# Kernel optimization log

Measured on AMD Instinct MI355X. Metric: run time of the kernel, lower is better.

The kernel has to match this reference:

```python
import jax, jax.numpy as jnp
import numpy as np

B, N, D, H = 4, 2048, 256, 8
d = D // H          # 32 per-head dim
EPS = 1e-5
SCALE = 1.0 / float(np.sqrt(d))


def setup_inputs() -> dict:
    key = jax.random.key(0)
    ks = jax.random.split(key, 6)
    s = 0.02
    x = jax.random.normal(ks[0], (B, N, D), jnp.float32)
    # RoPE frequencies: theta_j = 10000^(-2j/d), angle = pos * theta
    inv_freq = 1.0 / (10000.0 ** (jnp.arange(0, d, 2, dtype=jnp.float32) / d))  # (d/2,)
    ang = jnp.arange(N, dtype=jnp.float32)[:, None] * inv_freq[None, :]          # (N, d/2)
    return {
        "x": x,
        "freqs_cos": jnp.cos(ang),
        "freqs_sin": jnp.sin(ang),
        "w_qkv": jax.random.normal(ks[1], (D, 3 * D), jnp.float32) * s,
        "b_qkv": jnp.zeros((3 * D,), jnp.float32),
        "w_proj": jax.random.normal(ks[2], (D, D), jnp.float32) * s,
        "b_proj": jnp.zeros((D,), jnp.float32),
        "ln1_g": jnp.ones((D,), jnp.float32),
        "ln1_b": jnp.zeros((D,), jnp.float32),
        "ln2_g": jnp.ones((D,), jnp.float32),
        "ln2_b": jnp.zeros((D,), jnp.float32),
        "w1": jax.random.normal(ks[3], (D, 2 * D), jnp.float32) * s,
        "b1": jnp.zeros((2 * D,), jnp.float32),
        "w2": jax.random.normal(ks[4], (2 * D, D), jnp.float32) * s,
        "b2": jnp.zeros((D,), jnp.float32),
    }


def _layer_norm(x, g, b):
    mu = jnp.mean(x, axis=-1, keepdims=True)
    var = jnp.mean(jnp.square(x - mu), axis=-1, keepdims=True)
    return (x - mu) * jax.lax.rsqrt(var + EPS) * g + b


def _rope(t, cos, sin):
    # t: (B,H,N,d); interleaved (even,odd) pairs viewed as complex, multiplied by e^{i*ang}
    tr = t.reshape(B, H, N, d // 2, 2)
    te, to = tr[..., 0], tr[..., 1]
    c = cos[None, None, :, :]
    s = sin[None, None, :, :]
    oe = te * c - to * s
    oo = te * s + to * c
    return jnp.stack([oe, oo], axis=-1).reshape(B, H, N, d)


def reference(x, freqs_cos, freqs_sin, w_qkv, b_qkv, w_proj, b_proj,
              ln1_g, ln1_b, ln2_g, ln2_b, w1, b1, w2, b2):
    # Pre-LN MHSA with RoPE (dropout = identity at eval)
    h = _layer_norm(x, ln1_g, ln1_b)
    qkv = (h @ w_qkv + b_qkv).reshape(B, N, 3, H, d).transpose(0, 2, 3, 1, 4)  # (B,3,H,N,d)
    q, k, v = qkv[:, 0], qkv[:, 1], qkv[:, 2]
    q = _rope(q, freqs_cos, freqs_sin)
    k = _rope(k, freqs_cos, freqs_sin)
    attn = jax.nn.softmax(jnp.einsum('bhnd,bhmd->bhnm', q, k) * SCALE, axis=-1)
    out = jnp.einsum('bhnm,bhmd->bhnd', attn, v).transpose(0, 2, 1, 3).reshape(B, N, D)
    x = x + (out @ w_proj + b_proj)
    h = _layer_norm(x, ln2_g, ln2_b)
    ffn = jax.nn.relu(h @ w1 + b1) @ w2 + b2
    return x + ffn
```

## Files before the change

### kernel.cpp

```cpp
#include <hip/hip_runtime.h>
#include <hip/hip_bf16.h>
#include <math.h>

#define Bsz 4
#define Nseq 2048
#define Dm 256
#define Hh 8
#define Hd 32
#define EPS_ 1e-5f
#define SCALE_ 0.17677669529663687f
#define QSC_ (0.17677669529663687f * 1.4426950408889634f)

typedef __attribute__((ext_vector_type(8))) short short8;
typedef __attribute__((ext_vector_type(4))) short short4v;
typedef __attribute__((ext_vector_type(4))) float f32x4;
typedef __attribute__((ext_vector_type(16))) float f32x16;

__device__ __forceinline__ void gload16(const void* g, void* l) {
    __builtin_amdgcn_global_load_lds(
        (const __attribute__((address_space(1))) void*)g,
        (__attribute__((address_space(3))) void*)l, 16, 0, 0);
}

__device__ __forceinline__ short bf16s(float f) {
    __hip_bfloat16 h = __float2bfloat16(f);
    return *(short*)&h;
}

union FU { float f; unsigned u; };

__device__ __forceinline__ int pk2bf(float a, float b) {
    FU ua, ub; ua.f = a; ub.f = b;
    return (int)__builtin_amdgcn_perm(ub.u, ua.u, 0x07060302u);
}

union I4S8 { int i[4]; short8 s; };

__global__ __launch_bounds__(256) void prep_kernel(
    const float* __restrict__ x, const float* __restrict__ g1,
    const float* __restrict__ b1v, __hip_bfloat16* __restrict__ hout,
    const float* __restrict__ s0, const float* __restrict__ s1,
    const float* __restrict__ s2, const float* __restrict__ s3,
    __hip_bfloat16* __restrict__ d0, __hip_bfloat16* __restrict__ d1,
    __hip_bfloat16* __restrict__ d2, __hip_bfloat16* __restrict__ d3) {
    __shared__ float t[32][33];
    if (blockIdx.x < 2048) {
        int row  = blockIdx.x * 4 + (threadIdx.x >> 6);
        int lane = threadIdx.x & 63;
        const float* xr = x + (size_t)row * Dm;
        float4 v = *(const float4*)(xr + lane * 4);
        float s  = v.x + v.y + v.z + v.w;
        float ss = v.x * v.x + v.y * v.y + v.z * v.z + v.w * v.w;
        #pragma unroll
        for (int off = 32; off; off >>= 1) {
            s  += __shfl_xor(s, off);
            ss += __shfl_xor(ss, off);
        }
        float mu  = s * (1.0f / Dm);
        float var = ss * (1.0f / Dm) - mu * mu;
        float rs  = rsqrtf(var + EPS_);
        float4 gv = *(const float4*)(g1 + lane * 4);
        float4 bv = *(const float4*)(b1v + lane * 4);
        short4v o4 = { bf16s((v.x - mu) * rs * gv.x + bv.x),
                       bf16s((v.y - mu) * rs * gv.y + bv.y),
                       bf16s((v.z - mu) * rs * gv.z + bv.z),
                       bf16s((v.w - mu) * rs * gv.w + bv.w) };
        *(short4v*)(hout + (size_t)row * Dm + lane * 4) = o4;
        return;
    }
    int bid = blockIdx.x - 2048;
    const float* src; __hip_bfloat16* dst; int K, N, tb;
    if (bid < 192)      { src = s0; dst = d0; K = 256; N = 768; tb = bid; }
    else if (bid < 256) { src = s1; dst = d1; K = 256; N = 256; tb = bid - 192; }
    else if (bid < 384) { src = s2; dst = d2; K = 256; N = 512; tb = bid - 256; }
    else                { src = s3; dst = d3; K = 512; N = 256; tb = bid - 384; }
    int tn = N >> 5;
    int k0 = (tb / tn) * 32, n0 = (tb % tn) * 32;
    int c = threadIdx.x & 31, r0 = threadIdx.x >> 5;
    #pragma unroll
    for (int i = 0; i < 4; i++) {
        int r = r0 + i * 8;
        t[r][c] = src[(size_t)(k0 + r) * N + n0 + c];
    }
    __syncthreads();
    #pragma unroll
    for (int i = 0; i < 4; i++) {
        int n = r0 + i * 8;
        dst[(size_t)(n0 + n) * K + k0 + c] = __float2bfloat16(t[c][n]);
    }
}

__global__ __launch_bounds__(256) void qkv_mfma(const __hip_bfloat16* __restrict__ A,
                                                const __hip_bfloat16* __restrict__ Wt,
                                                const float* __restrict__ bias,
                                                const float* __restrict__ fcos,
                                                const float* __restrict__ fsin,
                                                __hip_bfloat16* __restrict__ qout,
                                                __hip_bfloat16* __restrict__ kout,
                                                __hip_bfloat16* __restrict__ vt) {
    const int K = 256;
    __shared__ __align__(16) __hip_bfloat16 As[2][64 * 64];
    __shared__ __align__(16) __hip_bfloat16 Bs[2][64 * 64];
    const int tid = threadIdx.x, w = tid >> 6, lane = tid & 63;
    const int lm = lane & 15, lq = lane >> 4;
    const int bm = blockIdx.y * 64, bn = blockIdx.x * 64;
    f32x4 acc[4];
    #pragma unroll
    for (int j = 0; j < 4; j++) acc[j] = (f32x4){0.f, 0.f, 0.f, 0.f};

    const int sr = tid >> 3, ssl = tid & 7;
    const int sgk = (ssl ^ (sr & 7)) * 8;
    const int sr2 = 32 + sr;
    const int sgk2 = (ssl ^ (sr2 & 7)) * 8;

    gload16(A + (size_t)(bm + sr) * K + sgk, &As[0][w * 512]);
    gload16(A + (size_t)(bm + sr2) * K + sgk2, &As[0][2048 + w * 512]);
    gload16(Wt + (size_t)(bn + sr) * K + sgk, &Bs[0][w * 512]);
    gload16(Wt + (size_t)(bn + sr2) * K + sgk2, &Bs[0][2048 + w * 512]);

    const int arow = w * 16 + lm;
    const int ar7 = arow & 7;
    for (int t = 0; t < K / 64; t++) {
        const int buf = t & 1;
        __syncthreads();
        if (t + 1 < K / 64) {
            int k0 = (t + 1) * 64;
            gload16(A + (size_t)(bm + sr) * K + k0 + sgk, &As[buf ^ 1][w * 512]);
            gload16(A + (size_t)(bm + sr2) * K + k0 + sgk2, &As[buf ^ 1][2048 + w * 512]);
            gload16(Wt + (size_t)(bn + sr) * K + k0 + sgk, &Bs[buf ^ 1][w * 512]);
            gload16(Wt + (size_t)(bn + sr2) * K + k0 + sgk2, &Bs[buf ^ 1][2048 + w * 512]);
        }
        #pragma unroll
        for (int ks = 0; ks < 2; ks++) {
            short8 a = *(const short8*)&As[buf][arow * 64 + (((ks * 4 + lq) ^ ar7) * 8)];
            #pragma unroll
            for (int nf = 0; nf < 4; nf++) {
                int cc = nf * 16 + lm;
                short8 bfr = *(const short8*)&Bs[buf][cc * 64 + (((ks * 4 + lq) ^ (cc & 7)) * 8)];
                acc[nf] = __builtin_amdgcn_mfma_f32_16x16x32_bf16(a, bfr, acc[nf], 0, 0, 0);
            }
        }
    }
    const int seg = bn >> 8;
    #pragma unroll
    for (int nf = 0; nf < 4; nf++) {
        int cg = bn + nf * 16 + lm;
        int hh = (cg & 255) >> 5;
        int dd = (nf & 1) * 16 + lm;
        int i0 = dd >> 1;
        float bi = bias[cg];
        #pragma unroll
        for (int r = 0; r < 4; r++) {
            int rg = bm + w * 16 + lq * 4 + r;
            int bb = rg >> 11, n = rg & (Nseq - 1);
            float v = acc[nf][r] + bi;
            if (seg == 2) {
                vt[(((size_t)(bb * Hh + hh)) * Hd + dd) * Nseq + n] = __float2bfloat16(v);
            } else {
                float vp = __shfl_xor(v, 1);
                float cs = fcos[n * 16 + i0], sn = fsin[n * 16 + i0];
                float outv = (dd & 1) ? (vp * sn + v * cs) : (v * cs - vp * sn);
                if (seg == 0) outv *= QSC_;
                __hip_bfloat16* dst = (seg == 0) ? qout : kout;
                dst[(((size_t)(bb * Hh + hh)) * Nseq + n) * Hd + dd] = __float2bfloat16(outv);
            }
        }
    }
}

__global__ __launch_bounds__(256) void attn_mfma(const __hip_bfloat16* __restrict__ q,
                                                 const __hip_bfloat16* __restrict__ k,
                                                 const __hip_bfloat16* __restrict__ vt,
                                                 __hip_bfloat16* __restrict__ att) {
    __shared__ __align__(16) char smem[4096 + 32768 + 512];
    __hip_bfloat16* Qs = (__hip_bfloat16*)smem;
    __hip_bfloat16* Vw = (__hip_bfloat16*)(smem + 4096);
    float* RedO = (float*)(smem + 4096);
    float* RedS = (float*)(smem + 4096 + 8192);
    float* smS  = (float*)(smem + 4096 + 8192 + 256);

    const int tid = threadIdx.x, w = tid >> 6, lane = tid & 63;
    const int l31 = lane & 31, hi = lane >> 5;
    const int wq = w >> 1, wk = w & 1;
    const int bh = blockIdx.y, qbase = blockIdx.x * 64;
    const __hip_bfloat16* qp = q + ((size_t)bh * Nseq + qbase) * Hd;
    const __hip_bfloat16* kp = k + (size_t)bh * Nseq * Hd;
    const __hip_bfloat16* vp = vt + (size_t)bh * Hd * Nseq;

    {
        int r = tid >> 2, sl = tid & 3;
        gload16(qp + r * 32 + ((sl ^ (r & 3)) * 8), Qs + w * 512);
    }
    __hip_bfloat16* myV = Vw + w * 4096;
    const int vd = (lane >> 3) & 7, vs = lane & 7;
    const int szv = (vs ^ vd) * 8;
    #pragma unroll
    for (int i = 0; i < 4; i++)
        gload16(vp + (size_t)(i * 8 + vd) * Nseq + wk * 64 + szv, myV + i * 512);
    const __hip_bfloat16* kb = kp + (size_t)wk * 64 * Hd + l31 * Hd + hi * 8;
    short8 kf0 = *(const short8*)(kb);
    short8 kf1 = *(const short8*)(kb + 16);
    short8 kf2 = *(const short8*)(kb + 1024);
    short8 kf3 = *(const short8*)(kb + 1040);
    __syncthreads();

    const int qrow = wq * 32 + l31;
    short8 qf0 = *(const short8*)&Qs[qrow * 32 + ((hi ^ (l31 & 3)) * 8)];
    short8 qf1 = *(const short8*)&Qs[qrow * 32 + (((2 + hi) ^ (l31 & 3)) * 8)];

    f32x16 O;
    #pragma unroll
    for (int i = 0; i < 16; i++) O[i] = 0.f;
    float sm = 0.f;

    for (int t = 0; t < 16; t++) {
        const int cur = t & 1;
        short8 nk0, nk1, nk2, nk3;
        if (t + 1 < 16) {
            const int c = 2 * (t + 1) + wk;
            asm volatile("s_waitcnt lgkmcnt(0)" ::: "memory");
            #pragma unroll
            for (int i = 0; i < 4; i++)
                gload16(vp + (size_t)(i * 8 + vd) * Nseq + c * 64 + szv,
                        myV + (cur ^ 1) * 2048 + i * 512);
            const __hip_bfloat16* kbn = kp + (size_t)c * 64 * Hd + l31 * Hd + hi * 8;
            nk0 = *(const short8*)(kbn);
            nk1 = *(const short8*)(kbn + 16);
            nk2 = *(const short8*)(kbn + 1024);
            nk3 = *(const short8*)(kbn + 1040);
        }
        f32x16 St0, St1;
        #pragma unroll
        for (int i = 0; i < 16; i++) { St0[i] = 0.f; St1[i] = 0.f; }
        St0 = __builtin_amdgcn_mfma_f32_32x32x16_bf16(kf0, qf0, St0, 0, 0, 0);
        St0 = __builtin_amdgcn_mfma_f32_32x32x16_bf16(kf1, qf1, St0, 0, 0, 0);
        St1 = __builtin_amdgcn_mfma_f32_32x32x16_bf16(kf2, qf0, St1, 0, 0, 0);
        St1 = __builtin_amdgcn_mfma_f32_32x32x16_bf16(kf3, qf1, St1, 0, 0, 0);
        int pk0[8], pk1[8];
        #pragma unroll
        for (int p = 0; p < 8; p++) {
            float a = __builtin_amdgcn_exp2f(St0[2 * p]);
            float b = __builtin_amdgcn_exp2f(St0[2 * p + 1]);
            sm += a + b;
            pk0[p] = pk2bf(a, b);
        }
        #pragma unroll
        for (int p = 0; p < 8; p++) {
            float a = __builtin_amdgcn_exp2f(St1[2 * p]);
            float b = __builtin_amdgcn_exp2f(St1[2 * p + 1]);
            sm += a + b;
            pk1[p] = pk2bf(a, b);
        }
        asm volatile("s_waitcnt vmcnt(8)" ::: "memory");
        #pragma unroll
        for (int tt = 0; tt < 4; tt++) {
            const int* PK = (tt >> 1) ? pk1 : pk0;
            const int base = 4 * (tt & 1);
            int keep0 = hi ? PK[base + 2] : PK[base + 0];
            int keep1 = hi ? PK[base + 3] : PK[base + 1];
            int send0 = hi ? PK[base + 0] : PK[base + 2];
            int send1 = hi ? PK[base + 1] : PK[base + 3];
            int x0 = __shfl_xor(send0, 32);
            int x1 = __shfl_xor(send1, 32);
            I4S8 u;
            u.i[0] = hi ? x0 : keep0;
            u.i[1] = hi ? x1 : keep1;
            u.i[2] = hi ? keep0 : x0;
            u.i[3] = hi ? keep1 : x1;
            short8 vf = *(const short8*)&myV[cur * 2048 + l31 * 64 +
                                            (((2 * tt + hi) ^ (l31 & 7)) * 8)];
            O = __builtin_amdgcn_mfma_f32_32x32x16_bf16(u.s, vf, O, 0, 0, 0);
        }
        if (t + 1 < 16) { kf0 = nk0; kf1 = nk1; kf2 = nk2; kf3 = nk3; }
    }
    sm += __shfl_xor(sm, 32);
    __syncthreads();
    if (wk == 1) {
        #pragma unroll
        for (int j = 0; j < 16; j++) RedO[(wq * 16 + j) * 64 + lane] = O[j];
        if (hi == 0) RedS[wq * 32 + l31] = sm;
    }
    __syncthreads();
    if (wk == 0) {
        #pragma unroll
        for (int j = 0; j < 16; j++) O[j] += RedO[(wq * 16 + j) * 64 + lane];
        sm += RedS[wq * 32 + l31];
        if (hi == 0) smS[wq * 32 + l31] = sm;
    }
    __syncthreads();
    if (wk == 0) {
        const int bb = bh >> 3, hh = bh & 7;
        #pragma unroll
        for (int m = 0; m < 4; m++) {
            float4 sv = *(const float4*)&smS[wq * 32 + 8 * m + 4 * hi];
            #pragma unroll
            for (int i = 0; i < 4; i++) {
                int n = qbase + wq * 32 + 8 * m + 4 * hi + i;
                att[((size_t)(bb * Nseq + n)) * Dm + hh * Hd + l31] =
                    __float2bfloat16(O[4 * m + i] * (1.0f / sv[i]));
            }
        }
    }
}

__global__ __launch_bounds__(256, 1) void tail_fused(
    const __hip_bfloat16* __restrict__ att, const __hip_bfloat16* __restrict__ wpT,
    const float* __restrict__ b_proj, const float* __restrict__ x,
    const float* __restrict__ g2, const float* __restrict__ bv2,
    const __hip_bfloat16* __restrict__ w1T, const float* __restrict__ b1,
    const __hip_bfloat16* __restrict__ w2T, const float* __restrict__ b2,
    float* __restrict__ out) {
    __shared__ __align__(16) __hip_bfloat16 WS[2][4][4096];
    __shared__ __align__(16) __hip_bfloat16 AH[8192];
    __shared__ __align__(16) __hip_bfloat16 PS[16384];
    __shared__ float red[4][32][2];
    __shared__ float muS[32], rsS[32];

    const int tid = threadIdx.x, w = tid >> 6, lane = tid & 63;
    const int lm = lane & 15, lq = lane >> 4;
    const int R0 = blockIdx.x * 32;
    const int c0 = w * 64;
    const int c0f = w * 128;

    {
        const int srow = tid >> 3, ssl = tid & 7;
        #pragma unroll
        for (int kt = 0; kt < 4; kt++)
            gload16(att + (size_t)(R0 + srow) * 256 + kt * 64 + ((ssl ^ (srow & 7)) * 8),
                    AH + kt * 2048 + w * 512);
    }
    #pragma unroll
    for (int ri = 0; ri < 8; ri++) {
        int r = ri * 8 + (lane >> 3), sl = lane & 7;
        gload16(wpT + (size_t)(c0 + r) * 256 + ((sl ^ (r & 7)) * 8), &WS[0][w][ri * 512]);
    }
    __syncthreads();

    short8 aF[2][4][2];
    #pragma unroll
    for (int mf = 0; mf < 2; mf++) {
        int r = mf * 16 + lm;
        #pragma unroll
        for (int kt = 0; kt < 4; kt++)
            #pragma unroll
            for (int ks = 0; ks < 2; ks++)
                aF[mf][kt][ks] = *(const short8*)&AH[kt * 2048 + r * 64 +
                                                    (((ks * 4 + lq) ^ (lm & 7)) * 8)];
    }
    float xr[2][4][4];
    #pragma unroll
    for (int mf = 0; mf < 2; mf++)
        #pragma unroll
        for (int r = 0; r < 4; r++) {
            int row = R0 + mf * 16 + lq * 4 + r;
            #pragma unroll
            for (int nf = 0; nf < 4; nf++)
                xr[mf][nf][r] = x[(size_t)row * 256 + c0 + nf * 16 + lm];
        }

    f32x4 acc[2][4];
    #pragma unroll
    for (int i = 0; i < 2; i++)
        #pragma unroll
        for (int j = 0; j < 4; j++) acc[i][j] = (f32x4){0.f, 0.f, 0.f, 0.f};
    for (int kt = 0; kt < 4; kt++) {
        const int buf = kt & 1;
        if (kt) __syncthreads();
        if (kt + 1 < 4) {
            #pragma unroll
            for (int ri = 0; ri < 8; ri++) {
                int r = ri * 8 + (lane >> 3), sl = lane & 7;
                gload16(wpT + (size_t)(c0 + r) * 256 + (kt + 1) * 64 + ((sl ^ (r & 7)) * 8),
                        &WS[buf ^ 1][w][ri * 512]);
            }
        }
        #pragma unroll
        for (int ks = 0; ks < 2; ks++)
            #pragma unroll
            for (int nf = 0; nf < 4; nf++) {
                int cc = nf * 16 + lm;
                short8 bfr = *(const short8*)&WS[buf][w][cc * 64 + (((ks * 4 + lq) ^ (lm & 7)) * 8)];
                #pragma unroll
                for (int mf = 0; mf < 2; mf++)
                    acc[mf][nf] = __builtin_amdgcn_mfma_f32_16x16x32_bf16(
                        aF[mf][kt][ks], bfr, acc[mf][nf], 0, 0, 0);
            }
    }
    #pragma unroll
    for (int nf = 0; nf < 4; nf++) {
        float bp = b_proj[c0 + nf * 16 + lm];
        #pragma unroll
        for (int mf = 0; mf < 2; mf++)
            #pragma unroll
            for (int r = 0; r < 4; r++) xr[mf][nf][r] += acc[mf][nf][r] + bp;
    }

    #pragma unroll
    for (int mf = 0; mf < 2; mf++)
        #pragma unroll
        for (int r = 0; r < 4; r++) {
            float s = 0.f, ss = 0.f;
            #pragma unroll
            for (int nf = 0; nf < 4; nf++) {
                float v = xr[mf][nf][r];
                s += v; ss += v * v;
            }
            #pragma unroll
            for (int off = 1; off <= 8; off <<= 1) {
                s  += __shfl_xor(s, off);
                ss += __shfl_xor(ss, off);
            }
            if (lm == 0) {
                int row = mf * 16 + lq * 4 + r;
                red[w][row][0] = s;
                red[w][row][1] = ss;
            }
        }
    #pragma unroll
    for (int ri = 0; ri < 8; ri++) {
        int r = ri * 16 + (lane >> 2), sl = lane & 3;
        gload16(w1T + (size_t)(c0f + r) * 256 + ((sl ^ (r & 3)) * 8), &WS[0][w][ri * 512]);
    }
    __syncthreads();
    if (tid < 32) {
        float s = red[0][tid][0] + red[1][tid][0] + red[2][tid][0] + red[3][tid][0];
        float ss = red[0][tid][1] + red[1][tid][1] + red[2][tid][1] + red[3][tid][1];
        float mu = s * (1.0f / 256.0f);
        muS[tid] = mu;
        rsS[tid] = rsqrtf(ss * (1.0f / 256.0f) - mu * mu + EPS_);
    }
    __syncthreads();
    #pragma unroll
    for (int mf = 0; mf < 2; mf++)
        #pragma unroll
        for (int r = 0; r < 4; r++) {
            int row = mf * 16 + lq * 4 + r;
            float mu = muS[row], rs = rsS[row];
            int rw7 = row & 7;
            #pragma unroll
            for (int nf = 0; nf < 4; nf++) {
                int c = c0 + nf * 16 + lm;
                float h = (xr[mf][nf][r] - mu) * rs * g2[c] + bv2[c];
                int slc = nf * 2 + (lm >> 3);
                AH[w * 2048 + row * 64 + ((slc ^ rw7) * 8) + (lm & 7)] = __float2bfloat16(h);
            }
        }
    __syncthreads();

    f32x4 acc2[2][8];
    #pragma unroll
    for (int i = 0; i < 2; i++)
        #pragma unroll
        for (int j = 0; j < 8; j++) acc2[i][j] = (f32x4){0.f, 0.f, 0.f, 0.f};
    for (int kt = 0; kt < 8; kt++) {
        const int buf = kt & 1;
        if (kt) __syncthreads();
        if (kt + 1 < 8) {
            #pragma unroll
            for (int ri = 0; ri < 8; ri++) {
                int r = ri * 16 + (lane >> 2), sl = lane & 3;
                gload16(w1T + (size_t)(c0f + r) * 256 + (kt + 1) * 32 + ((sl ^ (r & 3)) * 8),
                        &WS[buf ^ 1][w][ri * 512]);
            }
        }
        short8 aA[2];
        #pragma unroll
        for (int mf = 0; mf < 2; mf++) {
            int r = mf * 16 + lm;
            aA[mf] = *(const short8*)&AH[(kt >> 1) * 2048 + r * 64 +
                                         ((((kt & 1) * 4 + lq) ^ (lm & 7)) * 8)];
        }
        #pragma unroll
        for (int nf = 0; nf < 8; nf++) {
            int cc = nf * 16 + lm;
            short8 bfr = *(const short8*)&WS[buf][w][cc * 32 + ((lq ^ (lm & 3)) * 8)];
            #pragma unroll
            for (int mf = 0; mf < 2; mf++)
                acc2[mf][nf] = __builtin_amdgcn_mfma_f32_16x16x32_bf16(
                    aA[mf], bfr, acc2[mf][nf], 0, 0, 0);
        }
    }
    #pragma unroll
    for (int ri = 0; ri < 8; ri++) {
        int r = ri * 8 + (lane >> 3), sl = lane & 7;
        gload16(w2T + (size_t)(c0 + r) * 512 + ((sl ^ (r & 7)) * 8), &WS[0][w][ri * 512]);
    }
    #pragma unroll
    for (int nf = 0; nf < 8; nf++) {
        int c = c0f + nf * 16 + lm;
        float bb1 = b1[c];
        int kt8 = w * 2 + (nf >> 2);
        int slc = (nf & 3) * 2 + (lm >> 3);
        #pragma unroll
        for (int mf = 0; mf < 2; mf++)
            #pragma unroll
            for (int r = 0; r < 4; r++) {
                int row = mf * 16 + lq * 4 + r;
                float p = fmaxf(acc2[mf][nf][r] + bb1, 0.f);
                PS[kt8 * 2048 + row * 64 + ((slc ^ (row & 7)) * 8) + (lm & 7)] =
                    __float2bfloat16(p);
            }
    }
    __syncthreads();

    f32x4 acc3[2][4];
    #pragma unroll
    for (int i = 0; i < 2; i++)
        #pragma unroll
        for (int j = 0; j < 4; j++) acc3[i][j] = (f32x4){0.f, 0.f, 0.f, 0.f};
    for (int kt = 0; kt < 8; kt++) {
        const int buf = kt & 1;
        if (kt) __syncthreads();
        if (kt + 1 < 8) {
            #pragma unroll
            for (int ri = 0; ri < 8; ri++) {
                int r = ri * 8 + (lane >> 3), sl = lane & 7;
                gload16(w2T + (size_t)(c0 + r) * 512 + (kt + 1) * 64 + ((sl ^ (r & 7)) * 8),
                        &WS[buf ^ 1][w][ri * 512]);
            }
        }
        #pragma unroll
        for (int ks = 0; ks < 2; ks++) {
            short8 aP[2];
            #pragma unroll
            for (int mf = 0; mf < 2; mf++) {
                int r = mf * 16 + lm;
                aP[mf] = *(const short8*)&PS[kt * 2048 + r * 64 +
                                             (((ks * 4 + lq) ^ (lm & 7)) * 8)];
            }
            #pragma unroll
            for (int nf = 0; nf < 4; nf++) {
                int cc = nf * 16 + lm;
                short8 bfr = *(const short8*)&WS[buf][w][cc * 64 + (((ks * 4 + lq) ^ (lm & 7)) * 8)];
                #pragma unroll
                for (int mf = 0; mf < 2; mf++)
                    acc3[mf][nf] = __builtin_amdgcn_mfma_f32_16x16x32_bf16(
                        aP[mf], bfr, acc3[mf][nf], 0, 0, 0);
            }
        }
    }
    #pragma unroll
    for (int nf = 0; nf < 4; nf++) {
        int c = c0 + nf * 16 + lm;
        float bb2 = b2[c];
        #pragma unroll
        for (int mf = 0; mf < 2; mf++)
            #pragma unroll
            for (int r = 0; r < 4; r++) {
                int row = R0 + mf * 16 + lq * 4 + r;
                out[(size_t)row * 256 + c] = acc3[mf][nf][r] + bb2 + xr[mf][nf][r];
            }
    }
}

extern "C" void kernel_launch(void* const* d_in, const int* in_sizes, int n_in,
                              void* d_out, int out_size, void* d_ws, size_t ws_size,
                              hipStream_t stream) {
    const float* x      = (const float*)d_in[0];
    const float* fcos   = (const float*)d_in[1];
    const float* fsin   = (const float*)d_in[2];
    const float* w_qkv  = (const float*)d_in[3];
    const float* b_qkv  = (const float*)d_in[4];
    const float* w_proj = (const float*)d_in[5];
    const float* b_proj = (const float*)d_in[6];
    const float* ln1_g  = (const float*)d_in[7];
    const float* ln1_b  = (const float*)d_in[8];
    const float* ln2_g  = (const float*)d_in[9];
    const float* ln2_b  = (const float*)d_in[10];
    const float* w1     = (const float*)d_in[11];
    const float* b1     = (const float*)d_in[12];
    const float* w2     = (const float*)d_in[13];
    const float* b2     = (const float*)d_in[14];
    float* out = (float*)d_out;
    char* base = (char*)d_ws;
    const size_t MB = (size_t)1 << 20;

    __hip_bfloat16* h   = (__hip_bfloat16*)(base);
    __hip_bfloat16* qb  = (__hip_bfloat16*)(base + 4 * MB);
    __hip_bfloat16* kbf = (__hip_bfloat16*)(base + 8 * MB);
    __hip_bfloat16* vtb = (__hip_bfloat16*)(base + 12 * MB);
    __hip_bfloat16* att = (__hip_bfloat16*)(base + 16 * MB);
    __hip_bfloat16* wqT = (__hip_bfloat16*)(base + 20 * MB);
    __hip_bfloat16* wpT = (__hip_bfloat16*)(base + 20 * MB + 393216);
    __hip_bfloat16* w1T = (__hip_bfloat16*)(base + 20 * MB + 524288);
    __hip_bfloat16* w2T = (__hip_bfloat16*)(base + 20 * MB + 786432);

    prep_kernel<<<2560, 256, 0, stream>>>(x, ln1_g, ln1_b, h,
                                          w_qkv, w_proj, w1, w2, wqT, wpT, w1T, w2T);
    qkv_mfma<<<dim3(12, 128), 256, 0, stream>>>(h, wqT, b_qkv, fcos, fsin, qb, kbf, vtb);
    attn_mfma<<<dim3(Nseq / 64, Bsz * Hh), 256, 0, stream>>>(qb, kbf, vtb, att);
    tail_fused<<<256, 256, 0, stream>>>(att, wpT, b_proj, x, ln2_g, ln2_b,
                                        w1T, b1, w2T, b2, out);
}
```

Before: 169.4 us.

## Load Q and V fragments directly from global memory into registers in attention

```diff
diff --git a/kernel.cpp b/kernel.cpp
--- a/kernel.cpp
+++ b/kernel.cpp
@@ -172,12 +172,9 @@
                                                  const __hip_bfloat16* __restrict__ k,
                                                  const __hip_bfloat16* __restrict__ vt,
                                                  __hip_bfloat16* __restrict__ att) {
-    __shared__ __align__(16) char smem[4096 + 32768 + 512];
-    __hip_bfloat16* Qs = (__hip_bfloat16*)smem;
-    __hip_bfloat16* Vw = (__hip_bfloat16*)(smem + 4096);
-    float* RedO = (float*)(smem + 4096);
-    float* RedS = (float*)(smem + 4096 + 8192);
-    float* smS  = (float*)(smem + 4096 + 8192 + 256);
+    __shared__ float RedO[2048];
+    __shared__ float RedS[64];
+    __shared__ float smS[64];
 
     const int tid = threadIdx.x, w = tid >> 6, lane = tid & 63;
     const int l31 = lane & 31, hi = lane >> 5;
@@ -187,26 +184,21 @@
     const __hip_bfloat16* kp = k + (size_t)bh * Nseq * Hd;
     const __hip_bfloat16* vp = vt + (size_t)bh * Hd * Nseq;
 
-    {
-        int r = tid >> 2, sl = tid & 3;
-        gload16(qp + r * 32 + ((sl ^ (r & 3)) * 8), Qs + w * 512);
-    }
-    __hip_bfloat16* myV = Vw + w * 4096;
-    const int vd = (lane >> 3) & 7, vs = lane & 7;
-    const int szv = (vs ^ vd) * 8;
-    #pragma unroll
-    for (int i = 0; i < 4; i++)
-        gload16(vp + (size_t)(i * 8 + vd) * Nseq + wk * 64 + szv, myV + i * 512);
-    const __hip_bfloat16* kb = kp + (size_t)wk * 64 * Hd + l31 * Hd + hi * 8;
-    short8 kf0 = *(const short8*)(kb);
-    short8 kf1 = *(const short8*)(kb + 16);
-    short8 kf2 = *(const short8*)(kb + 1024);
-    short8 kf3 = *(const short8*)(kb + 1040);
-    __syncthreads();
-
-    const int qrow = wq * 32 + l31;
-    short8 qf0 = *(const short8*)&Qs[qrow * 32 + ((hi ^ (l31 & 3)) * 8)];
-    short8 qf1 = *(const short8*)&Qs[qrow * 32 + (((2 + hi) ^ (l31 & 3)) * 8)];
+    const __hip_bfloat16* qb2 = qp + (size_t)(wq * 32 + l31) * Hd + hi * 8;
+    short8 qf0 = *(const short8*)(qb2);
+    short8 qf1 = *(const short8*)(qb2 + 16);
+
+    const __hip_bfloat16* kb = kp + (size_t)l31 * Hd + hi * 8;
+    const __hip_bfloat16* vb = vp + (size_t)l31 * Nseq + hi * 8;
+
+    short8 kf0 = *(const short8*)(kb + wk * 2048);
+    short8 kf1 = *(const short8*)(kb + wk * 2048 + 16);
+    short8 kf2 = *(const short8*)(kb + wk * 2048 + 1024);
+    short8 kf3 = *(const short8*)(kb + wk * 2048 + 1040);
+    short8 vf0 = *(const short8*)(vb + wk * 64);
+    short8 vf1 = *(const short8*)(vb + wk * 64 + 16);
+    short8 vf2 = *(const short8*)(vb + wk * 64 + 32);
+    short8 vf3 = *(const short8*)(vb + wk * 64 + 48);
 
     f32x16 O;
     #pragma unroll
@@ -214,20 +206,19 @@
     float sm = 0.f;
 
     for (int t = 0; t < 16; t++) {
-        const int cur = t & 1;
-        short8 nk0, nk1, nk2, nk3;
+        short8 nk0, nk1, nk2, nk3, nv0, nv1, nv2, nv3;
         if (t + 1 < 16) {
             const int c = 2 * (t + 1) + wk;
-            asm volatile("s_waitcnt lgkmcnt(0)" ::: "memory");
-            #pragma unroll
-            for (int i = 0; i < 4; i++)
-                gload16(vp + (size_t)(i * 8 + vd) * Nseq + c * 64 + szv,
-                        myV + (cur ^ 1) * 2048 + i * 512);
-            const __hip_bfloat16* kbn = kp + (size_t)c * 64 * Hd + l31 * Hd + hi * 8;
+            const __hip_bfloat16* kbn = kb + (size_t)c * 2048;
+            const __hip_bfloat16* vbn = vb + c * 64;
             nk0 = *(const short8*)(kbn);
             nk1 = *(const short8*)(kbn + 16);
             nk2 = *(const short8*)(kbn + 1024);
             nk3 = *(const short8*)(kbn + 1040);
+            nv0 = *(const short8*)(vbn);
+            nv1 = *(const short8*)(vbn + 16);
+            nv2 = *(const short8*)(vbn + 32);
+            nv3 = *(const short8*)(vbn + 48);
         }
         f32x16 St0, St1;
         #pragma unroll
@@ -251,7 +242,6 @@
             sm += a + b;
             pk1[p] = pk2bf(a, b);
         }
-        asm volatile("s_waitcnt vmcnt(8)" ::: "memory");
         #pragma unroll
         for (int tt = 0; tt < 4; tt++) {
             const int* PK = (tt >> 1) ? pk1 : pk0;
@@ -267,14 +257,15 @@
             u.i[1] = hi ? x1 : keep1;
             u.i[2] = hi ? keep0 : x0;
             u.i[3] = hi ? keep1 : x1;
-            short8 vf = *(const short8*)&myV[cur * 2048 + l31 * 64 +
-                                            (((2 * tt + hi) ^ (l31 & 7)) * 8)];
+            short8 vf = (tt == 0) ? vf0 : (tt == 1) ? vf1 : (tt == 2) ? vf2 : vf3;
             O = __builtin_amdgcn_mfma_f32_32x32x16_bf16(u.s, vf, O, 0, 0, 0);
         }
-        if (t + 1 < 16) { kf0 = nk0; kf1 = nk1; kf2 = nk2; kf3 = nk3; }
+        if (t + 1 < 16) {
+            kf0 = nk0; kf1 = nk1; kf2 = nk2; kf3 = nk3;
+            vf0 = nv0; vf1 = nv1; vf2 = nv2; vf3 = nv3;
+        }
     }
     sm += __shfl_xor(sm, 32);
-    __syncthreads();
     if (wk == 1) {
         #pragma unroll
         for (int j = 0; j < 16; j++) RedO[(wq * 16 + j) * 64 + lane] = O[j];
```

Measured after the change: 177.7 us. 1.05x slower.

## Split attention keys four ways per block with 32-query tiles

Applied to the files above, without the earlier changes.

```diff
diff --git a/kernel.cpp b/kernel.cpp
--- a/kernel.cpp
+++ b/kernel.cpp
@@ -172,58 +172,50 @@
                                                  const __hip_bfloat16* __restrict__ k,
                                                  const __hip_bfloat16* __restrict__ vt,
                                                  __hip_bfloat16* __restrict__ att) {
-    __shared__ __align__(16) char smem[4096 + 32768 + 512];
+    __shared__ __align__(16) char smem[2048 + 16384 + 512];
     __hip_bfloat16* Qs = (__hip_bfloat16*)smem;
-    __hip_bfloat16* Vw = (__hip_bfloat16*)(smem + 4096);
-    float* RedO = (float*)(smem + 4096);
-    float* RedS = (float*)(smem + 4096 + 8192);
-    float* smS  = (float*)(smem + 4096 + 8192 + 256);
+    __hip_bfloat16* Vw = (__hip_bfloat16*)(smem + 2048);
+    float* RedO = (float*)(smem + 2048);
+    float* RedS = (float*)(smem + 2048 + 16384);
+    float* smS  = (float*)(smem + 2048 + 16384 + 384);
 
     const int tid = threadIdx.x, w = tid >> 6, lane = tid & 63;
     const int l31 = lane & 31, hi = lane >> 5;
-    const int wq = w >> 1, wk = w & 1;
-    const int bh = blockIdx.y, qbase = blockIdx.x * 64;
+    const int bh = blockIdx.y, qbase = blockIdx.x * 32;
     const __hip_bfloat16* qp = q + ((size_t)bh * Nseq + qbase) * Hd;
     const __hip_bfloat16* kp = k + (size_t)bh * Nseq * Hd;
     const __hip_bfloat16* vp = vt + (size_t)bh * Hd * Nseq;
 
-    {
+    if (w < 2) {
         int r = tid >> 2, sl = tid & 3;
         gload16(qp + r * 32 + ((sl ^ (r & 3)) * 8), Qs + w * 512);
     }
-    __hip_bfloat16* myV = Vw + w * 4096;
+    __hip_bfloat16* myV = Vw + w * 2048;
     const int vd = (lane >> 3) & 7, vs = lane & 7;
     const int szv = (vs ^ vd) * 8;
     #pragma unroll
     for (int i = 0; i < 4; i++)
-        gload16(vp + (size_t)(i * 8 + vd) * Nseq + wk * 64 + szv, myV + i * 512);
-    const __hip_bfloat16* kb = kp + (size_t)wk * 64 * Hd + l31 * Hd + hi * 8;
-    short8 kf0 = *(const short8*)(kb);
-    short8 kf1 = *(const short8*)(kb + 16);
-    short8 kf2 = *(const short8*)(kb + 1024);
-    short8 kf3 = *(const short8*)(kb + 1040);
-    __syncthreads();
-
-    const int qrow = wq * 32 + l31;
-    short8 qf0 = *(const short8*)&Qs[qrow * 32 + ((hi ^ (l31 & 3)) * 8)];
-    short8 qf1 = *(const short8*)&Qs[qrow * 32 + (((2 + hi) ^ (l31 & 3)) * 8)];
+        gload16(vp + (size_t)(i * 8 + vd) * Nseq + w * 64 + szv, myV + i * 512);
+    const __hip_bfloat16* kb = kp + (size_t)l31 * Hd + hi * 8;
+    short8 kf0 = *(const short8*)(kb + w * 2048);
+    short8 kf1 = *(const short8*)(kb + w * 2048 + 16);
+    short8 kf2 = *(const short8*)(kb + w * 2048 + 1024);
+    short8 kf3 = *(const short8*)(kb + w * 2048 + 1040);
+    __syncthreads();
+
+    short8 qf0 = *(const short8*)&Qs[l31 * 32 + ((hi ^ (l31 & 3)) * 8)];
+    short8 qf1 = *(const short8*)&Qs[l31 * 32 + (((2 + hi) ^ (l31 & 3)) * 8)];
 
     f32x16 O;
     #pragma unroll
     for (int i = 0; i < 16; i++) O[i] = 0.f;
     float sm = 0.f;
 
-    for (int t = 0; t < 16; t++) {
-        const int cur = t & 1;
+    for (int t = 0; t < 8; t++) {
         short8 nk0, nk1, nk2, nk3;
-        if (t + 1 < 16) {
-            const int c = 2 * (t + 1) + wk;
-            asm volatile("s_waitcnt lgkmcnt(0)" ::: "memory");
-            #pragma unroll
-            for (int i = 0; i < 4; i++)
-                gload16(vp + (size_t)(i * 8 + vd) * Nseq + c * 64 + szv,
-                        myV + (cur ^ 1) * 2048 + i * 512);
-            const __hip_bfloat16* kbn = kp + (size_t)c * 64 * Hd + l31 * Hd + hi * 8;
+        if (t + 1 < 8) {
+            const int c = 4 * (t + 1) + w;
+            const __hip_bfloat16* kbn = kb + (size_t)c * 2048;
             nk0 = *(const short8*)(kbn);
             nk1 = *(const short8*)(kbn + 16);
             nk2 = *(const short8*)(kbn + 1024);
@@ -251,7 +243,8 @@
             sm += a + b;
             pk1[p] = pk2bf(a, b);
         }
-        asm volatile("s_waitcnt vmcnt(8)" ::: "memory");
+        if (t + 1 < 8) asm volatile("s_waitcnt vmcnt(4)" ::: "memory");
+        else           asm volatile("s_waitcnt vmcnt(0)" ::: "memory");
         #pragma unroll
         for (int tt = 0; tt < 4; tt++) {
             const int* PK = (tt >> 1) ? pk1 : pk0;
@@ -267,35 +260,44 @@
             u.i[1] = hi ? x1 : keep1;
             u.i[2] = hi ? keep0 : x0;
             u.i[3] = hi ? keep1 : x1;
-            short8 vf = *(const short8*)&myV[cur * 2048 + l31 * 64 +
-                                            (((2 * tt + hi) ^ (l31 & 7)) * 8)];
+            short8 vf = *(const short8*)&myV[l31 * 64 + (((2 * tt + hi) ^ (l31 & 7)) * 8)];
             O = __builtin_amdgcn_mfma_f32_32x32x16_bf16(u.s, vf, O, 0, 0, 0);
         }
-        if (t + 1 < 16) { kf0 = nk0; kf1 = nk1; kf2 = nk2; kf3 = nk3; }
+        if (t + 1 < 8) {
+            asm volatile("s_waitcnt lgkmcnt(0)" ::: "memory");
+            const int c = 4 * (t + 1) + w;
+            #pragma unroll
+            for (int i = 0; i < 4; i++)
+                gload16(vp + (size_t)(i * 8 + vd) * Nseq + c * 64 + szv, myV + i * 512);
+            kf0 = nk0; kf1 = nk1; kf2 = nk2; kf3 = nk3;
+        }
     }
     sm += __shfl_xor(sm, 32);
     __syncthreads();
-    if (wk == 1) {
-        #pragma unroll
-        for (int j = 0; j < 16; j++) RedO[(wq * 16 + j) * 64 + lane] = O[j];
-        if (hi == 0) RedS[wq * 32 + l31] = sm;
-    }
-    __syncthreads();
-    if (wk == 0) {
-        #pragma unroll
-        for (int j = 0; j < 16; j++) O[j] += RedO[(wq * 16 + j) * 64 + lane];
-        sm += RedS[wq * 32 + l31];
-        if (hi == 0) smS[wq * 32 + l31] = sm;
-    }
-    __syncthreads();
-    if (wk == 0) {
+    if (w) {
+        #pragma unroll
+        for (int j = 0; j < 16; j++) RedO[(w - 1) * 1024 + j * 64 + lane] = O[j];
+        if (hi == 0) RedS[(w - 1) * 32 + l31] = sm;
+    }
+    __syncthreads();
+    if (w == 0) {
+        #pragma unroll
+        for (int j = 0; j < 16; j++)
+            O[j] += RedO[j * 64 + lane] + RedO[1024 + j * 64 + lane] +
+                    RedO[2048 + j * 64 + lane];
+        sm += RedS[l31] + RedS[32 + l31] + RedS[64 + l31];
+        if (hi == 0) smS[l31] = sm;
+        __builtin_amdgcn_s_waitcnt(0);
+    }
+    __syncthreads();
+    if (w == 0) {
         const int bb = bh >> 3, hh = bh & 7;
         #pragma unroll
         for (int m = 0; m < 4; m++) {
-            float4 sv = *(const float4*)&smS[wq * 32 + 8 * m + 4 * hi];
+            float4 sv = *(const float4*)&smS[8 * m + 4 * hi];
             #pragma unroll
             for (int i = 0; i < 4; i++) {
-                int n = qbase + wq * 32 + 8 * m + 4 * hi + i;
+                int n = qbase + 8 * m + 4 * hi + i;
                 att[((size_t)(bb * Nseq + n)) * Dm + hh * Hd + l31] =
                     __float2bfloat16(O[4 * m + i] * (1.0f / sv[i]));
             }
@@ -588,7 +590,7 @@
     prep_kernel<<<2560, 256, 0, stream>>>(x, ln1_g, ln1_b, h,
                                           w_qkv, w_proj, w1, w2, wqT, wpT, w1T, w2T);
     qkv_mfma<<<dim3(12, 128), 256, 0, stream>>>(h, wqT, b_qkv, fcos, fsin, qb, kbf, vtb);
-    attn_mfma<<<dim3(Nseq / 64, Bsz * Hh), 256, 0, stream>>>(qb, kbf, vtb, att);
+    attn_mfma<<<dim3(Nseq / 32, Bsz * Hh), 256, 0, stream>>>(qb, kbf, vtb, att);
     tail_fused<<<256, 256, 0, stream>>>(att, wpT, b_proj, x, ln2_g, ln2_b,
                                         w1T, b1, w2T, b2, out);
 }
```

Result: no change. 166.3 us (-1.8%).
